# Kernel optimization log

Measured on AMD Instinct MI355X. Metric: run time of the kernel, lower is better.

Reference implementation:

```python
import jax, jax.numpy as jnp
import numpy as np

N_NODES = 100000
N_EDGES = 1600000
IN_DIM = 128
HID2 = 128   # hidden_dim * 2
OUT_DIM = 1


def setup_inputs() -> dict:
    key = jax.random.key(0)
    ks = jax.random.split(key, 9)
    x = jax.random.normal(ks[0], (N_NODES, IN_DIM), dtype=jnp.float32)
    edge_index = jax.random.randint(ks[1], (2, N_EDGES), 0, N_NODES, dtype=jnp.int32)
    s_in = 1.0 / np.sqrt(IN_DIM)
    s_h = 1.0 / np.sqrt(HID2)
    W_conv = jax.random.normal(ks[2], (IN_DIM, HID2), dtype=jnp.float32) * s_in
    b_conv = jnp.zeros((HID2,), dtype=jnp.float32)
    W_proj = jax.random.normal(ks[3], (IN_DIM, HID2), dtype=jnp.float32) * s_in
    b_proj = jax.random.normal(ks[4], (HID2,), dtype=jnp.float32) * s_in
    W_out = jax.random.normal(ks[5], (HID2, OUT_DIM), dtype=jnp.float32) * s_h
    b_out = jax.random.normal(ks[6], (OUT_DIM,), dtype=jnp.float32) * s_h
    return {"x": x, "edge_index": edge_index, "W_conv": W_conv, "b_conv": b_conv,
            "W_proj": W_proj, "b_proj": b_proj, "W_out": W_out, "b_out": b_out}


def reference(x, edge_index, W_conv, b_conv, W_proj, b_proj, W_out, b_out):
    n = x.shape[0]
    loops = jnp.arange(n, dtype=edge_index.dtype)
    self_loops = jnp.stack([loops, loops])  # [2, N]
    # self loops added twice: once in forward() explicitly, once inside GCNConv (default)
    ei = jnp.concatenate([edge_index, self_loops, self_loops], axis=1)
    row, col = ei[0], ei[1]  # source -> destination
    # symmetric GCN normalization: deg computed over destinations
    deg = jax.ops.segment_sum(jnp.ones_like(row, dtype=x.dtype), col, num_segments=n)
    dinv = jnp.where(deg > 0, deg ** -0.5, 0.0)
    norm = dinv[row] * dinv[col]  # [E']
    xw = x @ W_conv  # [N, HID2]
    msgs = xw[row] * norm[:, None]  # [E', HID2] gather + scale
    conv = jax.ops.segment_sum(msgs, col, num_segments=n) + b_conv
    combined = jax.nn.relu(conv + x @ W_proj + b_proj)
    out = combined @ W_out + b_out  # [N, 1]
    return out.squeeze()
```

## Files before the change

### kernel.cpp

```cpp
#include <hip/hip_runtime.h>

#define N_NODES 100000
#define N_EDGES 1600000
#define DIM 128
#define NBIN 256
#define WINSZ 391
#define SLOT 64
#define CH 2048
#define NP1 ((N_EDGES + CH - 1) / CH)
#define SUBCAP 32
#define NGEMM ((N_NODES + 63) / 64)
#define SENT 0xFFFFFFFFu

typedef __attribute__((ext_vector_type(8))) short short8;
typedef __attribute__((ext_vector_type(4))) float f32x4;
typedef __attribute__((ext_vector_type(2))) float f32x2;

__device__ inline unsigned short bf16u(float f) {
    unsigned u = __builtin_bit_cast(unsigned, f);
    return (unsigned short)((u + 0x7FFFu + ((u >> 16) & 1u)) >> 16);
}
__device__ inline unsigned pk_bf16(float a, float b) {
    return (unsigned)bf16u(a) | ((unsigned)bf16u(b) << 16);
}
__device__ inline float bf16_lo(unsigned v) { return __builtin_bit_cast(float, v << 16); }
__device__ inline float bf16_hi(unsigned v) { return __builtin_bit_cast(float, v & 0xFFFF0000u); }

__device__ inline unsigned pk_fp8x4(float a, float b, float c, float d) {
    int lo = __builtin_amdgcn_cvt_pk_fp8_f32(a, b, 0, false);
    int hi = __builtin_amdgcn_cvt_pk_fp8_f32(c, d, lo, true);
    return (unsigned)hi;
}

#if __has_builtin(__builtin_amdgcn_cvt_pk_f32_fp8)
__device__ inline f32x2 pkcvt_lo(unsigned v) {
    return __builtin_amdgcn_cvt_pk_f32_fp8(v, false);
}
__device__ inline f32x2 pkcvt_hi(unsigned v) {
    return __builtin_amdgcn_cvt_pk_f32_fp8(v, true);
}
#else
__device__ inline f32x2 pkcvt_lo(unsigned v) {
    f32x2 r;
    r.x = __builtin_amdgcn_cvt_f32_fp8((int)v, 0);
    r.y = __builtin_amdgcn_cvt_f32_fp8((int)v, 1);
    return r;
}
__device__ inline f32x2 pkcvt_hi(unsigned v) {
    f32x2 r;
    r.x = __builtin_amdgcn_cvt_f32_fp8((int)v, 2);
    r.y = __builtin_amdgcn_cvt_f32_fp8((int)v, 3);
    return r;
}
#endif


__launch_bounds__(512)
__global__ void k_prep(const float* __restrict__ Wc, const float* __restrict__ Wp,
                       const int* __restrict__ erow, const int* __restrict__ ecol,
                       int* __restrict__ cntT, unsigned* __restrict__ gbin,
                       unsigned short* __restrict__ WtG) {
    const int tid = threadIdx.x;
    if (blockIdx.x >= NP1) {
        int idx = (blockIdx.x - NP1) * 512 + tid;
        int n = idx >> 7, k = idx & 127;
        float v = (n < 128) ? Wc[k * 128 + n] : Wp[k * 128 + (n - 128)];
        int t = n >> 4, mm = n & 15;
        int q = k >> 5, qd = (k >> 3) & 3, j = k & 7;
        WtG[(((t * 4 + q) * 64 + qd * 16 + mm) << 3) + j] = bf16u(v);
        return;
    }
    __shared__ int lcnt[NBIN];
    const int blk = blockIdx.x;
    if (tid < NBIN) lcnt[tid] = 0;
    __syncthreads();
    const int e0 = blk * CH;
    const int e1 = (e0 + CH < N_EDGES) ? e0 + CH : N_EDGES;
    for (int e = e0 + tid; e < e1; e += 512) {
        int c = ecol[e];
        int bin = c / WINSZ;
        unsigned pay = (unsigned)erow[e] | ((unsigned)(c - bin * WINSZ) << 17);
        int r = atomicAdd(&lcnt[bin], 1);
        if (r < SUBCAP) gbin[((size_t)blk * NBIN + bin) * SUBCAP + r] = pay;
    }
    __syncthreads();
    if (tid < NBIN) {
        int v = lcnt[tid];
        cntT[blk * NBIN + tid] = (v < SUBCAP) ? v : SUBCAP;
    }
}

__launch_bounds__(1024)
__global__ void k_bins(const int* __restrict__ cntT,
                       const unsigned* __restrict__ gbin,
                       int* __restrict__ srcb2,
                       int* __restrict__ cnt,
                       float* __restrict__ dinv) {
    __shared__ int lcnt[WINSZ];
    __shared__ int cl[NP1];
    const int tid = threadIdx.x;
    const int bin = blockIdx.x;
    const int lo  = bin * WINSZ;
    const int nw  = (lo + WINSZ < N_NODES) ? WINSZ : (N_NODES - lo);
    if (nw <= 0) return;
    for (int i = tid; i < WINSZ; i += 1024) lcnt[i] = 0;
    for (int i = tid; i < NP1; i += 1024) cl[i] = cntT[i * NBIN + bin];
    __syncthreads();

    const int g = tid >> 5;
    const int lidx = tid & 31;

    int sg = g;
    int len = cl[sg];
    const unsigned* seg = gbin + ((size_t)sg * NBIN + bin) * SUBCAP;
    unsigned p0 = (lidx < len) ? seg[lidx] : SENT;

    while (sg < NP1) {
        const int nsg = sg + 32;
        const unsigned* nseg = seg;
        unsigned n0 = SENT;
        if (nsg < NP1) {
            int nlen = cl[nsg];
            nseg = gbin + ((size_t)nsg * NBIN + bin) * SUBCAP;
            n0 = (lidx < nlen) ? nseg[lidx] : SENT;
        }
        if (p0 != SENT) {
            int row = p0 & 0x1FFFF, c = p0 >> 17;
            int r = atomicAdd(&lcnt[c], 1);
            if (r < SLOT) srcb2[((lo + c) << 6) + r] = row;
        }
        sg = nsg; seg = nseg; p0 = n0;
    }
    __syncthreads();
    for (int i = tid; i < nw; i += 1024) {
        int v = lcnt[i];
        cnt[lo + i]  = (v < SLOT) ? v : SLOT;
        dinv[lo + i] = rsqrtf((float)(v + 2));
    }
}

__launch_bounds__(256)
__global__ void k_gemm(const float* __restrict__ x,
                       const unsigned short* __restrict__ WtG,
                       const float* __restrict__ bc,
                       const float* __restrict__ bp,
                       const float* __restrict__ dinv,
                       unsigned* __restrict__ xwb8,
                       unsigned* __restrict__ accb) {
    __shared__ alignas(16) unsigned short wbuf[16384];

    const int tid   = threadIdx.x;
    const int node0 = blockIdx.x * 64;
    const int w     = tid >> 6;
    const int lane  = tid & 63;
    const int m     = lane & 15;
    const int quad  = lane >> 4;

    const uint4* gsrc = (const uint4*)WtG;
    uint4*       lbuf = (uint4*)wbuf;

    #pragma unroll
    for (int i = 0; i < 8; ++i) lbuf[i * 256 + tid] = gsrc[i * 256 + tid];

    const int  rowg  = node0 + w * 16 + m;
    const bool valid = rowg < N_NODES;
    const float* xrow = x + (size_t)rowg * DIM;

    short8 afr[4];
    #pragma unroll
    for (int q = 0; q < 4; q++) {
        float4 xa = make_float4(0.f, 0.f, 0.f, 0.f);
        float4 xb = make_float4(0.f, 0.f, 0.f, 0.f);
        if (valid) {
            xa = *(const float4*)(xrow + 32 * q + 8 * quad);
            xb = *(const float4*)(xrow + 32 * q + 8 * quad + 4);
        }
        uint4 pa;
        pa.x = pk_bf16(xa.x, xa.y); pa.y = pk_bf16(xa.z, xa.w);
        pa.z = pk_bf16(xb.x, xb.y); pa.w = pk_bf16(xb.z, xb.w);
        afr[q] = __builtin_bit_cast(short8, pa);
    }

    float bias[8];
    #pragma unroll
    for (int p = 0; p < 4; p++) {
        bias[2 * p]     = bc[32 * p + m]      + bp[32 * p + m];
        bias[2 * p + 1] = bc[32 * p + m + 16] + bp[32 * p + m + 16];
    }

    __syncthreads();

    f32x4 acc0[8];
    #pragma unroll
    for (int t = 0; t < 8; ++t) {
        f32x4 a = (f32x4){0.f, 0.f, 0.f, 0.f};
        #pragma unroll
        for (int q = 0; q < 4; ++q) {
            short8 bfrag = *(const short8*)(wbuf + (((t * 4 + q) * 64 + lane) << 3));
            a = __builtin_amdgcn_mfma_f32_16x16x32_bf16(afr[q], bfrag, a, 0, 0, 0);
        }
        acc0[t] = a;
    }

    #pragma unroll
    for (int r = 0; r < 4; ++r) {
        int node = node0 + w * 16 + quad * 4 + r;
        if (node < N_NODES) {
            float dv = dinv[node];
            uint2 xv;
            xv.x = pk_fp8x4(acc0[0][r] * dv, acc0[1][r] * dv,
                            acc0[2][r] * dv, acc0[3][r] * dv);
            xv.y = pk_fp8x4(acc0[4][r] * dv, acc0[5][r] * dv,
                            acc0[6][r] * dv, acc0[7][r] * dv);
            *(uint2*)(xwb8 + (size_t)node * 32 + m * 2) = xv;
        }
    }

    __syncthreads();

    #pragma unroll
    for (int i = 0; i < 8; ++i) lbuf[i * 256 + tid] = gsrc[2048 + i * 256 + tid];

    __syncthreads();

    f32x4 acc1[8];
    #pragma unroll
    for (int t = 0; t < 8; ++t) {
        f32x4 a = (f32x4){0.f, 0.f, 0.f, 0.f};
        #pragma unroll
        for (int q = 0; q < 4; ++q) {
            short8 bfrag = *(const short8*)(wbuf + (((t * 4 + q) * 64 + lane) << 3));
            a = __builtin_amdgcn_mfma_f32_16x16x32_bf16(afr[q], bfrag, a, 0, 0, 0);
        }
        acc1[t] = a;
    }

    #pragma unroll
    for (int r = 0; r < 4; ++r) {
        int node = node0 + w * 16 + quad * 4 + r;
        if (node < N_NODES) {
            uint4 pv;
            pv.x = pk_bf16(acc1[0][r] + bias[0], acc1[1][r] + bias[1]);
            pv.y = pk_bf16(acc1[2][r] + bias[2], acc1[3][r] + bias[3]);
            pv.z = pk_bf16(acc1[4][r] + bias[4], acc1[5][r] + bias[5]);
            pv.w = pk_bf16(acc1[6][r] + bias[6], acc1[7][r] + bias[7]);
            *(uint4*)(accb + (size_t)node * 64 + m * 4) = pv;
        }
    }
}

__launch_bounds__(256)
__global__ void k_gather_final(const int* __restrict__ srcb2,
                               const int* __restrict__ cnt,
                               const float* __restrict__ dinv,
                               const unsigned* __restrict__ xw32,
                               const unsigned* __restrict__ accb,
                               const float* __restrict__ wout,
                               const float* __restrict__ bout,
                               float* __restrict__ out) {
    int t = blockIdx.x * 256 + threadIdx.x;
    int node = t >> 6;
    int lane = t & 63;
    if (node >= N_NODES) return;

    const int d  = lane & 31;
    const int eh = lane >> 5;
    const int* sp = srcb2 + (node << 6);

    int4 ia = *(const int4*)sp;
    int4 ib = *(const int4*)(sp + 4);
    unsigned vs = xw32[((unsigned)node << 5) | d];
    uint2 av = *(const uint2*)(accb + ((unsigned)node << 6) + 2u * ((unsigned)d));
    float ddst = dinv[node];
    int c = cnt[node];

    f32x2 a01 = (f32x2){0.f, 0.f};
    f32x2 a23 = (f32x2){0.f, 0.f};

    int j = 0;
    for (; j + 8 <= c; ) {
        const int jn = j + 8;
        const bool more = jn + 8 <= c;
        int4 na, nb;
        if (more) {
            na = *(const int4*)(sp + jn);
            nb = *(const int4*)(sp + jn + 4);
        }
        int r0 = eh ? ia.y : ia.x;
        int r1 = eh ? ia.w : ia.z;
        int r2 = eh ? ib.y : ib.x;
        int r3 = eh ? ib.w : ib.z;
        unsigned v0 = xw32[((unsigned)r0 << 5) | d];
        unsigned v1 = xw32[((unsigned)r1 << 5) | d];
        unsigned v2 = xw32[((unsigned)r2 << 5) | d];
        unsigned v3 = xw32[((unsigned)r3 << 5) | d];
        a01 += pkcvt_lo(v0); a23 += pkcvt_hi(v0);
        a01 += pkcvt_lo(v1); a23 += pkcvt_hi(v1);
        a01 += pkcvt_lo(v2); a23 += pkcvt_hi(v2);
        a01 += pkcvt_lo(v3); a23 += pkcvt_hi(v3);
        j = jn;
        if (more) { ia = na; ib = nb; }
    }
    if (j < c) {
        const int mx = c - 1;
        int p0 = j + eh, p1 = j + 2 + eh, p2 = j + 4 + eh, p3 = j + 6 + eh;
        int r0 = sp[(p0 < mx) ? p0 : mx];
        int r1 = sp[(p1 < mx) ? p1 : mx];
        int r2 = sp[(p2 < mx) ? p2 : mx];
        int r3 = sp[(p3 < mx) ? p3 : mx];
        unsigned v0 = xw32[((unsigned)r0 << 5) | d];
        unsigned v1 = xw32[((unsigned)r1 << 5) | d];
        unsigned v2 = xw32[((unsigned)r2 << 5) | d];
        unsigned v3 = xw32[((unsigned)r3 << 5) | d];
        if (p0 >= c) v0 = 0u;
        if (p1 >= c) v1 = 0u;
        if (p2 >= c) v2 = 0u;
        if (p3 >= c) v3 = 0u;
        a01 += pkcvt_lo(v0); a23 += pkcvt_hi(v0);
        a01 += pkcvt_lo(v1); a23 += pkcvt_hi(v1);
        a01 += pkcvt_lo(v2); a23 += pkcvt_hi(v2);
        a01 += pkcvt_lo(v3); a23 += pkcvt_hi(v3);
    }

    a01.x += __shfl_down(a01.x, 32);
    a01.y += __shfl_down(a01.y, 32);
    a23.x += __shfl_down(a23.x, 32);
    a23.y += __shfl_down(a23.y, 32);

    f32x2 sl0 = pkcvt_lo(vs), sl1 = pkcvt_hi(vs);
    float s0 = a01.x + 2.f * sl0.x;
    float s1 = a01.y + 2.f * sl0.y;
    float s2 = a23.x + 2.f * sl1.x;
    float s3 = a23.y + 2.f * sl1.y;

    float v0 = bf16_lo(av.x) + ddst * s0;
    float v1 = bf16_hi(av.x) + ddst * s1;
    float v2 = bf16_lo(av.y) + ddst * s2;
    float v3 = bf16_hi(av.y) + ddst * s3;

    int f00 = 64 * (d & 1) + (d >> 1);
    float r = fmaxf(v0, 0.f) * wout[f00]
            + fmaxf(v1, 0.f) * wout[f00 + 16]
            + fmaxf(v2, 0.f) * wout[f00 + 32]
            + fmaxf(v3, 0.f) * wout[f00 + 48];
    #pragma unroll
    for (int off = 16; off > 0; off >>= 1) r += __shfl_down(r, off);
    if (lane == 0) out[node] = r + bout[0];
}

extern "C" void kernel_launch(void* const* d_in, const int* in_sizes, int n_in,
                              void* d_out, int out_size, void* d_ws, size_t ws_size,
                              hipStream_t stream) {
    const float* x      = (const float*)d_in[0];
    const int*   ei     = (const int*)  d_in[1];
    const float* W_conv = (const float*)d_in[2];
    const float* b_conv = (const float*)d_in[3];
    const float* W_proj = (const float*)d_in[4];
    const float* b_proj = (const float*)d_in[5];
    const float* W_out  = (const float*)d_in[6];
    const float* b_out  = (const float*)d_in[7];
    float* out = (float*)d_out;

    const int* e_row = ei;
    const int* e_col = ei + N_EDGES;

    char* p = (char*)d_ws;
    unsigned*       xwb8  = (unsigned*)p;       p += (size_t)N_NODES * 32 * 4;
    unsigned*       accb  = (unsigned*)p;       p += (size_t)N_NODES * 64 * 4;
    int*            srcb2 = (int*)p;            p += (size_t)N_NODES * SLOT * 4;
    int*            cntT  = (int*)p;            p += (size_t)NP1 * NBIN * 4;
    int*            cnt   = (int*)p;            p += (size_t)N_NODES * 4;
    float*          dinv  = (float*)p;          p += (size_t)N_NODES * 4;
    unsigned short* WtG   = (unsigned short*)p; p += 256 * 128 * 2;
    unsigned*       gbin  = xwb8;

    k_prep<<<NP1 + 64, 512, 0, stream>>>(W_conv, W_proj, e_row, e_col, cntT, gbin, WtG);
    k_bins<<<NBIN, 1024, 0, stream>>>(cntT, gbin, srcb2, cnt, dinv);
    k_gemm<<<NGEMM, 256, 0, stream>>>(x, WtG, b_conv, b_proj, dinv, xwb8, accb);
    k_gather_final<<<(N_NODES * 64 + 255) / 256, 256, 0, stream>>>(
        srcb2, cnt, dinv, xwb8, accb, W_out, b_out, out);
}
```

Measured before the change: 193.0 us.

## Split fp8 feature table into two halves and gather in two passes

The GEMM now writes the scaled fp8 conv features into two separate 64-byte-per-node tables (low and high feature halves) instead of one 128-byte table. The gather/final kernel is launched twice, once per half. Each pass gathers from only one table, and the second pass adds its partial output dot product into the result. The intent is to shrink the random-gather working set so more of it stays in cache. In exchange, the edge index lists, counts and dinv are read twice, there is an extra launch, and the second pass does a read-modify-write on the output.

```diff
diff --git a/kernel.cpp b/kernel.cpp
--- a/kernel.cpp
+++ b/kernel.cpp
@@ -145,7 +145,8 @@
                        const float* __restrict__ bc,
                        const float* __restrict__ bp,
                        const float* __restrict__ dinv,
-                       unsigned* __restrict__ xwb8,
+                       unsigned* __restrict__ xlo,
+                       unsigned* __restrict__ xhi,
                        unsigned* __restrict__ accb) {
     __shared__ alignas(16) unsigned short wbuf[16384];
 
@@ -202,17 +203,21 @@
         acc0[t] = a;
     }
 
-    #pragma unroll
-    for (int r = 0; r < 4; ++r) {
-        int node = node0 + w * 16 + quad * 4 + r;
-        if (node < N_NODES) {
-            float dv = dinv[node];
-            uint2 xv;
-            xv.x = pk_fp8x4(acc0[0][r] * dv, acc0[1][r] * dv,
-                            acc0[2][r] * dv, acc0[3][r] * dv);
-            xv.y = pk_fp8x4(acc0[4][r] * dv, acc0[5][r] * dv,
-                            acc0[6][r] * dv, acc0[7][r] * dv);
-            *(uint2*)(xwb8 + (size_t)node * 32 + m * 2) = xv;
+    {
+        unsigned* tab  = (m < 8) ? xlo : xhi;
+        const int dbase = (m < 8) ? (m << 1) : ((m - 8) << 1);
+        #pragma unroll
+        for (int r = 0; r < 4; ++r) {
+            int node = node0 + w * 16 + quad * 4 + r;
+            if (node < N_NODES) {
+                float dv = dinv[node];
+                uint2 xv;
+                xv.x = pk_fp8x4(acc0[0][r] * dv, acc0[1][r] * dv,
+                                acc0[2][r] * dv, acc0[3][r] * dv);
+                xv.y = pk_fp8x4(acc0[4][r] * dv, acc0[5][r] * dv,
+                                acc0[6][r] * dv, acc0[7][r] * dv);
+                *(uint2*)(tab + ((size_t)node << 4) + dbase) = xv;
+            }
         }
     }
 
@@ -250,27 +255,28 @@
 }
 
 __launch_bounds__(256)
-__global__ void k_gather_final(const int* __restrict__ srcb2,
-                               const int* __restrict__ cnt,
-                               const float* __restrict__ dinv,
-                               const unsigned* __restrict__ xw32,
-                               const unsigned* __restrict__ accb,
-                               const float* __restrict__ wout,
-                               const float* __restrict__ bout,
-                               float* __restrict__ out) {
+__global__ void k_gather_half(const int* __restrict__ srcb2,
+                              const int* __restrict__ cnt,
+                              const float* __restrict__ dinv,
+                              const unsigned* __restrict__ tab,
+                              const unsigned* __restrict__ accb,
+                              const float* __restrict__ wout,
+                              const float* __restrict__ bout,
+                              float* __restrict__ out,
+                              const int half) {
     int t = blockIdx.x * 256 + threadIdx.x;
     int node = t >> 6;
     int lane = t & 63;
     if (node >= N_NODES) return;
 
-    const int d  = lane & 31;
-    const int eh = lane >> 5;
+    const int d_ = lane & 15;
+    const int g  = lane >> 4;
     const int* sp = srcb2 + (node << 6);
 
     int4 ia = *(const int4*)sp;
     int4 ib = *(const int4*)(sp + 4);
-    unsigned vs = xw32[((unsigned)node << 5) | d];
-    uint2 av = *(const uint2*)(accb + ((unsigned)node << 6) + 2u * ((unsigned)d));
+    unsigned vs = tab[((unsigned)node << 4) | d_];
+    uint2 av = *(const uint2*)(accb + ((unsigned)node << 6) + (half << 5) + 2u * d_);
     float ddst = dinv[node];
     int c = cnt[node];
 
@@ -286,46 +292,36 @@
             na = *(const int4*)(sp + jn);
             nb = *(const int4*)(sp + jn + 4);
         }
-        int r0 = eh ? ia.y : ia.x;
-        int r1 = eh ? ia.w : ia.z;
-        int r2 = eh ? ib.y : ib.x;
-        int r3 = eh ? ib.w : ib.z;
-        unsigned v0 = xw32[((unsigned)r0 << 5) | d];
-        unsigned v1 = xw32[((unsigned)r1 << 5) | d];
-        unsigned v2 = xw32[((unsigned)r2 << 5) | d];
-        unsigned v3 = xw32[((unsigned)r3 << 5) | d];
+        int r0 = (g == 0) ? ia.x : (g == 1) ? ia.z : (g == 2) ? ib.x : ib.z;
+        int r1 = (g == 0) ? ia.y : (g == 1) ? ia.w : (g == 2) ? ib.y : ib.w;
+        unsigned v0 = tab[((unsigned)r0 << 4) | d_];
+        unsigned v1 = tab[((unsigned)r1 << 4) | d_];
         a01 += pkcvt_lo(v0); a23 += pkcvt_hi(v0);
         a01 += pkcvt_lo(v1); a23 += pkcvt_hi(v1);
-        a01 += pkcvt_lo(v2); a23 += pkcvt_hi(v2);
-        a01 += pkcvt_lo(v3); a23 += pkcvt_hi(v3);
         j = jn;
         if (more) { ia = na; ib = nb; }
     }
     if (j < c) {
         const int mx = c - 1;
-        int p0 = j + eh, p1 = j + 2 + eh, p2 = j + 4 + eh, p3 = j + 6 + eh;
+        int p0 = j + 2 * g, p1 = p0 + 1;
         int r0 = sp[(p0 < mx) ? p0 : mx];
         int r1 = sp[(p1 < mx) ? p1 : mx];
-        int r2 = sp[(p2 < mx) ? p2 : mx];
-        int r3 = sp[(p3 < mx) ? p3 : mx];
-        unsigned v0 = xw32[((unsigned)r0 << 5) | d];
-        unsigned v1 = xw32[((unsigned)r1 << 5) | d];
-        unsigned v2 = xw32[((unsigned)r2 << 5) | d];
-        unsigned v3 = xw32[((unsigned)r3 << 5) | d];
+        unsigned v0 = tab[((unsigned)r0 << 4) | d_];
+        unsigned v1 = tab[((unsigned)r1 << 4) | d_];
         if (p0 >= c) v0 = 0u;
         if (p1 >= c) v1 = 0u;
-        if (p2 >= c) v2 = 0u;
-        if (p3 >= c) v3 = 0u;
         a01 += pkcvt_lo(v0); a23 += pkcvt_hi(v0);
         a01 += pkcvt_lo(v1); a23 += pkcvt_hi(v1);
-        a01 += pkcvt_lo(v2); a23 += pkcvt_hi(v2);
-        a01 += pkcvt_lo(v3); a23 += pkcvt_hi(v3);
     }
 
     a01.x += __shfl_down(a01.x, 32);
     a01.y += __shfl_down(a01.y, 32);
     a23.x += __shfl_down(a23.x, 32);
     a23.y += __shfl_down(a23.y, 32);
+    a01.x += __shfl_down(a01.x, 16);
+    a01.y += __shfl_down(a01.y, 16);
+    a23.x += __shfl_down(a23.x, 16);
+    a23.y += __shfl_down(a23.y, 16);
 
     f32x2 sl0 = pkcvt_lo(vs), sl1 = pkcvt_hi(vs);
     float s0 = a01.x + 2.f * sl0.x;
@@ -338,14 +334,18 @@
     float v2 = bf16_lo(av.y) + ddst * s2;
     float v3 = bf16_hi(av.y) + ddst * s3;
 
+    int d = (half << 4) | d_;
     int f00 = 64 * (d & 1) + (d >> 1);
     float r = fmaxf(v0, 0.f) * wout[f00]
             + fmaxf(v1, 0.f) * wout[f00 + 16]
             + fmaxf(v2, 0.f) * wout[f00 + 32]
             + fmaxf(v3, 0.f) * wout[f00 + 48];
     #pragma unroll
-    for (int off = 16; off > 0; off >>= 1) r += __shfl_down(r, off);
-    if (lane == 0) out[node] = r + bout[0];
+    for (int off = 8; off > 0; off >>= 1) r += __shfl_down(r, off);
+    if (lane == 0) {
+        if (half == 0) out[node] = r + bout[0];
+        else           out[node] += r;
+    }
 }
 
 extern "C" void kernel_launch(void* const* d_in, const int* in_sizes, int n_in,
@@ -365,18 +365,21 @@
     const int* e_col = ei + N_EDGES;
 
     char* p = (char*)d_ws;
-    unsigned*       xwb8  = (unsigned*)p;       p += (size_t)N_NODES * 32 * 4;
+    unsigned*       xlo   = (unsigned*)p;       p += (size_t)N_NODES * 16 * 4;
+    unsigned*       xhi   = (unsigned*)p;       p += (size_t)N_NODES * 16 * 4;
     unsigned*       accb  = (unsigned*)p;       p += (size_t)N_NODES * 64 * 4;
     int*            srcb2 = (int*)p;            p += (size_t)N_NODES * SLOT * 4;
     int*            cntT  = (int*)p;            p += (size_t)NP1 * NBIN * 4;
     int*            cnt   = (int*)p;            p += (size_t)N_NODES * 4;
     float*          dinv  = (float*)p;          p += (size_t)N_NODES * 4;
     unsigned short* WtG   = (unsigned short*)p; p += 256 * 128 * 2;
-    unsigned*       gbin  = xwb8;
+    unsigned*       gbin  = xlo;
 
     k_prep<<<NP1 + 64, 512, 0, stream>>>(W_conv, W_proj, e_row, e_col, cntT, gbin, WtG);
     k_bins<<<NBIN, 1024, 0, stream>>>(cntT, gbin, srcb2, cnt, dinv);
-    k_gemm<<<NGEMM, 256, 0, stream>>>(x, WtG, b_conv, b_proj, dinv, xwb8, accb);
-    k_gather_final<<<(N_NODES * 64 + 255) / 256, 256, 0, stream>>>(
-        srcb2, cnt, dinv, xwb8, accb, W_out, b_out, out);
-}
+    k_gemm<<<NGEMM, 256, 0, stream>>>(x, WtG, b_conv, b_proj, dinv, xlo, xhi, accb);
+    k_gather_half<<<(N_NODES * 64 + 255) / 256, 256, 0, stream>>>(
+        srcb2, cnt, dinv, xlo, accb, W_out, b_out, out, 0);
+    k_gather_half<<<(N_NODES * 64 + 255) / 256, 256, 0, stream>>>(
+        srcb2, cnt, dinv, xhi, accb, W_out, b_out, out, 1);
+}
```

Result: slower. 234.5 us (+21.5%).
